# Kernel tuning notes

Measured on AMD Instinct MI355X. Metric: run time of the kernel, lower is better.

## Reference

```python
import jax, jax.numpy as jnp
import numpy as np

N = 8192
IN_F = 512
OUT_F = 128
NUM_CLASSES = 10
ALPHA = 0.2  # LeakyReLU negative slope
NEG_INF = -9e15


def setup_inputs() -> dict:
    key = jax.random.key(0)
    k_h, k_d, k_W, k_a, k_cw, k_cb = jax.random.split(key, 6)
    h = jax.random.normal(k_h, (N, IN_F), dtype=jnp.float32)
    dist = jax.random.randint(k_d, (N, N), 0, 2, dtype=jnp.int32)
    # xavier_uniform with gain=1.414
    gain = 1.414
    lim_W = gain * np.sqrt(6.0 / (IN_F + OUT_F))
    W = jax.random.uniform(k_W, (IN_F, OUT_F), minval=-lim_W, maxval=lim_W, dtype=jnp.float32)
    lim_a = gain * np.sqrt(6.0 / (2 * OUT_F + 1))
    a = jax.random.uniform(k_a, (2 * OUT_F, 1), minval=-lim_a, maxval=lim_a, dtype=jnp.float32)
    # nn.Linear(out_features, num_classes): weight [C, out], bias [C]
    lim_c = np.sqrt(1.0 / OUT_F)
    Wc = jax.random.uniform(k_cw, (NUM_CLASSES, OUT_F), minval=-lim_c, maxval=lim_c, dtype=jnp.float32)
    bc = jax.random.uniform(k_cb, (NUM_CLASSES,), minval=-lim_c, maxval=lim_c, dtype=jnp.float32)
    return {"h": h, "dist": dist, "W": W, "a": a, "Wc": Wc, "bc": bc}


def reference(h, dist, W, a, Wc, bc):
    Wh = h @ W                              # [N, out]
    Wh1 = Wh @ a[:OUT_F]                    # [N, 1]
    Wh2 = Wh @ a[OUT_F:]                    # [N, 1]
    e = jax.nn.leaky_relu(Wh1 + Wh2.T, negative_slope=ALPHA)  # [N, N]
    att = jnp.where(dist > 0, e, NEG_INF)
    att = jax.nn.softmax(att, axis=1)       # [N, N]
    h_update = jax.nn.elu(att @ Wh)         # [N, out] (dropout inactive at inference)
    y_pred = h_update @ Wc.T + bc           # [N, num_classes]
    return y_pred
```

## Files before the change

### kernel.cpp

```cpp
#include <hip/hip_runtime.h>
#include <stdint.h>

#define N 8192
#define IN_F 512
#define OUT_F 128
#define NCLS 10
#define ALPHA 0.2f

typedef float f32x4 __attribute__((ext_vector_type(4)));
typedef int   i32x4 __attribute__((ext_vector_type(4)));
typedef short s16x4 __attribute__((ext_vector_type(4)));
typedef short s16x8 __attribute__((ext_vector_type(8)));

__device__ __forceinline__ short f2bf(float x) {
    unsigned u = __builtin_bit_cast(unsigned, x);
    u = (u + 0x7FFFu + ((u >> 16) & 1u)) >> 16;
    return (short)u;
}
__device__ __forceinline__ float bf2f(short s) {
    unsigned u = ((unsigned)(unsigned short)s) << 16;
    return __builtin_bit_cast(float, u);
}

__global__ void split_w_kernel(const float* __restrict__ W,
                               short* __restrict__ WThi, short* __restrict__ WTlo) {
    int idx = blockIdx.x * 256 + threadIdx.x;
    int k = idx >> 7, col = idx & 127;
    float x = W[idx];
    short hi = f2bf(x);
    short lo = f2bf(x - bf2f(hi));
    size_t a = (size_t)(k >> 5) * (128 * 32) + (size_t)col * 32 + (k & 31);
    WThi[a] = hi;
    WTlo[a] = lo;
}

#define WH_ROWS 16
#define WH_STR 520

__global__ __launch_bounds__(256, 2)
void wh_kernel(const float* __restrict__ h, const short* __restrict__ WThi,
               const short* __restrict__ WTlo, const float* __restrict__ a,
               short* __restrict__ WhT, float* __restrict__ Wh1,
               float* __restrict__ Wh2) {
    __shared__ __align__(16) short Ahi[WH_ROWS][WH_STR];
    __shared__ __align__(16) short Alo[WH_ROWS][WH_STR];
    __shared__ __align__(16) float whs[WH_ROWS][OUT_F + 4];

    const int t = threadIdx.x;
    const int r0 = blockIdx.x * WH_ROWS;

    {
        int row = t >> 4, c4 = t & 15;
        const float* hrow = h + (size_t)(r0 + row) * IN_F;
        #pragma unroll
        for (int jj = 0; jj < 4; ++jj) {
            int k0 = c4 * 8 + jj * 128;
            f32x4 x0 = *(const f32x4*)(hrow + k0);
            f32x4 x1 = *(const f32x4*)(hrow + k0 + 4);
            s16x8 hi, lo;
            #pragma unroll
            for (int e = 0; e < 4; ++e) {
                short h0 = f2bf(x0[e]); hi[e] = h0; lo[e] = f2bf(x0[e] - bf2f(h0));
                short h1 = f2bf(x1[e]); hi[4 + e] = h1; lo[4 + e] = f2bf(x1[e] - bf2f(h1));
            }
            *(s16x8*)&Ahi[row][k0] = hi;
            *(s16x8*)&Alo[row][k0] = lo;
        }
    }
    __syncthreads();

    const int lane = t & 63, w = t >> 6;
    const int q = lane >> 4, ln16 = lane & 15;
    f32x4 acc[2] = {};
    #pragma unroll
    for (int kc = 0; kc < IN_F / 32; ++kc) {
        s16x8 ahi = *(const s16x8*)&Ahi[ln16][kc * 32 + q * 8];
        s16x8 alo = *(const s16x8*)&Alo[ln16][kc * 32 + q * 8];
        #pragma unroll
        for (int nt = 0; nt < 2; ++nt) {
            int col = w * 32 + nt * 16 + ln16;
            size_t boff = (size_t)kc * 4096 + (size_t)col * 32 + q * 8;
            s16x8 bhi = *(const s16x8*)(WThi + boff);
            s16x8 blo = *(const s16x8*)(WTlo + boff);
            acc[nt] = __builtin_amdgcn_mfma_f32_16x16x32_bf16(ahi, bhi, acc[nt], 0, 0, 0);
            acc[nt] = __builtin_amdgcn_mfma_f32_16x16x32_bf16(ahi, blo, acc[nt], 0, 0, 0);
            acc[nt] = __builtin_amdgcn_mfma_f32_16x16x32_bf16(alo, bhi, acc[nt], 0, 0, 0);
        }
    }
    #pragma unroll
    for (int nt = 0; nt < 2; ++nt)
        #pragma unroll
        for (int reg = 0; reg < 4; ++reg)
            whs[q * 4 + reg][w * 32 + nt * 16 + ln16] = acc[nt][reg];
    __syncthreads();

    if (t < 128) {
        int r = t >> 3, s = t & 7;
        float s1 = 0.f, s2 = 0.f;
        #pragma unroll
        for (int cc = 0; cc < 16; ++cc) {
            int c = s * 16 + cc;
            float v = whs[r][c];
            s1 = fmaf(v, a[c], s1);
            s2 = fmaf(v, a[OUT_F + c], s2);
        }
        s1 += __shfl_xor(s1, 1); s1 += __shfl_xor(s1, 2); s1 += __shfl_xor(s1, 4);
        s2 += __shfl_xor(s2, 1); s2 += __shfl_xor(s2, 2); s2 += __shfl_xor(s2, 4);
        if (s == 0) { Wh1[r0 + r] = s1; Wh2[r0 + r] = s2; }
    }

    {
        int c = t >> 1, h8 = t & 1;
        s16x8 pack;
        #pragma unroll
        for (int rr = 0; rr < 8; ++rr) pack[rr] = f2bf(whs[h8 * 8 + rr][c]);
        size_t addr = (size_t)(r0 >> 5) * 4096 + (size_t)c * 32 + (r0 & 16) + h8 * 8;
        *(s16x8*)(WhT + addr) = pack;
    }
}

#define BM 32
#define BK 256
#define ASTR (BK + 8)

__global__ __launch_bounds__(256, 4)
void attn_kernel(const int* __restrict__ dist, const short* __restrict__ WhT,
                 const float* __restrict__ Wh1v, const float* __restrict__ Wh2v,
                 float* __restrict__ acc_part, float* __restrict__ l_part,
                 int nit) {
    __shared__ __align__(16) short As[2][BM][ASTR];

    const int t = threadIdx.x;
    const int it = blockIdx.x & 255;
    const int sp = blockIdx.x >> 8;
    const int i0 = it * BM;
    const int r = t >> 3, s = t & 7;
    const int lane = t & 63, w = t >> 6;
    const int q = lane >> 4, ln16 = lane & 15;
    const int j0 = sp * nit * BK;

    const int* __restrict__ drow = dist + (size_t)(i0 + r) * N + j0;
    const float* __restrict__ wh2p = Wh2v + j0;
    const float wh1 = Wh1v[i0 + r];
    float l_acc = 0.f;
    f32x4 acc[2][2] = {};

    i32x4 d[8];
    #pragma unroll
    for (int u = 0; u < 8; ++u) d[u] = *(const i32x4*)(drow + u * 32 + s * 4);

    for (int kt = 0; kt < nit; ++kt) {
        const int jb = kt * BK;
        const bool more = (kt + 1) < nit;
        i32x4 dn[8];
        if (more) {
            #pragma unroll
            for (int u = 0; u < 8; ++u)
                dn[u] = *(const i32x4*)(drow + jb + BK + u * 32 + s * 4);
        }
        short* arow = &As[kt & 1][r][0];
        #pragma unroll
        for (int u = 0; u < 8; ++u) {
            f32x4 w2 = *(const f32x4*)(wh2p + jb + u * 32 + s * 4);
            s16x4 pk;
            #pragma unroll
            for (int e = 0; e < 4; ++e) {
                float sv = wh1 + w2[e];
                float lr = fmaxf(sv, ALPHA * sv);
                float pv = (d[u][e] > 0) ? __expf(lr) : 0.f;
                l_acc += pv;
                pk[e] = f2bf(pv);
            }
            *(s16x4*)(arow + u * 32 + s * 4) = pk;
        }
        __syncthreads();
        const short* ab = &As[kt & 1][0][0];
        const short* bbase = WhT + (size_t)(j0 + jb) * 128;
        #pragma unroll
        for (int kc = 0; kc < BK / 32; ++kc) {
            s16x8 a0 = *(const s16x8*)(ab + ln16 * ASTR + kc * 32 + q * 8);
            s16x8 a1 = *(const s16x8*)(ab + (16 + ln16) * ASTR + kc * 32 + q * 8);
            #pragma unroll
            for (int nt = 0; nt < 2; ++nt) {
                int col = w * 32 + nt * 16 + ln16;
                s16x8 b = *(const s16x8*)(bbase + (size_t)kc * 4096 + col * 32 + q * 8);
                acc[0][nt] = __builtin_amdgcn_mfma_f32_16x16x32_bf16(a0, b, acc[0][nt], 0, 0, 0);
                acc[1][nt] = __builtin_amdgcn_mfma_f32_16x16x32_bf16(a1, b, acc[1][nt], 0, 0, 0);
            }
        }
        if (more) {
            #pragma unroll
            for (int u = 0; u < 8; ++u) d[u] = dn[u];
        }
    }

    l_acc += __shfl_xor(l_acc, 1);
    l_acc += __shfl_xor(l_acc, 2);
    l_acc += __shfl_xor(l_acc, 4);
    if (s == 0) l_part[(size_t)sp * N + i0 + r] = l_acc;

    float* ap = acc_part + (size_t)sp * N * OUT_F + (size_t)i0 * OUT_F;
    #pragma unroll
    for (int mt = 0; mt < 2; ++mt)
        #pragma unroll
        for (int reg = 0; reg < 4; ++reg) {
            int row = mt * 16 + q * 4 + reg;
            #pragma unroll
            for (int nt = 0; nt < 2; ++nt)
                ap[(size_t)row * OUT_F + w * 32 + nt * 16 + ln16] = acc[mt][nt][reg];
        }
}

__global__ __launch_bounds__(256, 4)
void reduce_kernel(const float* __restrict__ acc_part, const float* __restrict__ l_part,
                   const float* __restrict__ Wc, const float* __restrict__ bcv,
                   float* __restrict__ out, int split) {
    __shared__ __align__(16) float hu[16][OUT_F + 4];
    const int t = threadIdx.x;
    const int i0 = blockIdx.x * 16;
    const int row = t >> 4, cg = t & 15;

    f32x4 v0 = {0.f, 0.f, 0.f, 0.f}, v1 = {0.f, 0.f, 0.f, 0.f};
    float l = 0.f;
    for (int s = 0; s < split; ++s) {
        const float* ap = acc_part + (size_t)s * N * OUT_F + (size_t)(i0 + row) * OUT_F + cg * 8;
        v0 += *(const f32x4*)ap;
        v1 += *(const f32x4*)(ap + 4);
        l += l_part[(size_t)s * N + i0 + row];
    }
    float inv = 1.f / l;
    #pragma unroll
    for (int e = 0; e < 4; ++e) {
        float x0 = v0[e] * inv; x0 = x0 > 0.f ? x0 : (__expf(x0) - 1.f);
        float x1 = v1[e] * inv; x1 = x1 > 0.f ? x1 : (__expf(x1) - 1.f);
        hu[row][cg * 8 + e] = x0;
        hu[row][cg * 8 + 4 + e] = x1;
    }
    __syncthreads();

    if (t < 16 * NCLS) {
        int rr = t / NCLS, cls = t - rr * NCLS;
        const f32x4* hurow = (const f32x4*)&hu[rr][0];
        const f32x4* wcrow = (const f32x4*)(Wc + cls * OUT_F);
        float sum = bcv[cls];
        #pragma unroll 8
        for (int c4 = 0; c4 < OUT_F / 4; ++c4) {
            f32x4 hv = hurow[c4];
            f32x4 wv = wcrow[c4];
            sum += hv[0] * wv[0] + hv[1] * wv[1] + hv[2] * wv[2] + hv[3] * wv[3];
        }
        out[(size_t)(i0 + rr) * NCLS + cls] = sum;
    }
}

extern "C" void kernel_launch(void* const* d_in, const int* in_sizes, int n_in,
                              void* d_out, int out_size, void* d_ws, size_t ws_size,
                              hipStream_t stream) {
    const float* h    = (const float*)d_in[0];
    const int*   dist = (const int*)d_in[1];
    const float* W    = (const float*)d_in[2];
    const float* a    = (const float*)d_in[3];
    const float* Wc   = (const float*)d_in[4];
    const float* bc   = (const float*)d_in[5];
    float* out = (float*)d_out;

    char* ws = (char*)d_ws;
    size_t off = 0;
    short* WhT  = (short*)(ws + off); off += (size_t)OUT_F * N * 2;
    short* WThi = (short*)(ws + off); off += (size_t)IN_F * OUT_F * 2;
    short* WTlo = (short*)(ws + off); off += (size_t)IN_F * OUT_F * 2;
    float* Wh1  = (float*)(ws + off); off += (size_t)N * 4;
    float* Wh2  = (float*)(ws + off); off += (size_t)N * 4;

    size_t per_split = (size_t)N * OUT_F * 4 + (size_t)N * 4;
    int split = 4;
    if (off + 4 * per_split > ws_size) split = 2;
    if (off + 2 * per_split > ws_size) split = 1;
    float* acc_part = (float*)(ws + off); off += (size_t)split * N * OUT_F * 4;
    float* l_part   = (float*)(ws + off);

    hipLaunchKernelGGL(split_w_kernel, dim3(256), dim3(256), 0, stream, W, WThi, WTlo);
    hipLaunchKernelGGL(wh_kernel, dim3(N / WH_ROWS), dim3(256), 0, stream,
                       h, WThi, WTlo, a, WhT, Wh1, Wh2);
    int nit = N / (BK * split);
    hipLaunchKernelGGL(attn_kernel, dim3(256 * split), dim3(256), 0, stream,
                       dist, WhT, Wh1, Wh2, acc_part, l_part, nit);
    hipLaunchKernelGGL(reduce_kernel, dim3(N / 16), dim3(256), 0, stream,
                       acc_part, l_part, Wc, bc, out, split);
}
```

Measured before the change: 441.7 us.

## Compute attention A fragments directly in registers, dropping LDS staging

The attention kernel now has each lane load the dist and Wh2 values matching its MFMA A-fragment layout and compute exp weights straight into registers. This removes the LDS tile, the __syncthreads, and the LDS reads. Each wave now owns 16 rows and all 128 output columns (8 accumulators), with a 64-row block tile, BK of 128 and a split-K of 8. The cost is losing the dist prefetch and double buffering, each wave reading the full WhT slice itself, and more partial sums for the reduce kernel.

```diff
diff --git a/kernel.cpp b/kernel.cpp
--- a/kernel.cpp
+++ b/kernel.cpp
@@ -119,96 +119,81 @@
     }
 }
 
-#define BM 32
-#define BK 256
-#define ASTR (BK + 8)
+#define BK 128
 
 __global__ __launch_bounds__(256, 4)
 void attn_kernel(const int* __restrict__ dist, const short* __restrict__ WhT,
                  const float* __restrict__ Wh1v, const float* __restrict__ Wh2v,
                  float* __restrict__ acc_part, float* __restrict__ l_part,
                  int nit) {
-    __shared__ __align__(16) short As[2][BM][ASTR];
-
     const int t = threadIdx.x;
-    const int it = blockIdx.x & 255;
-    const int sp = blockIdx.x >> 8;
-    const int i0 = it * BM;
-    const int r = t >> 3, s = t & 7;
+    const int it = blockIdx.x & 127;
+    const int sp = blockIdx.x >> 7;
+    const int i0 = it * 64;
     const int lane = t & 63, w = t >> 6;
-    const int q = lane >> 4, ln16 = lane & 15;
+    const int q = lane >> 4, m = lane & 15;
+    const int row = i0 + w * 16 + m;
     const int j0 = sp * nit * BK;
 
-    const int* __restrict__ drow = dist + (size_t)(i0 + r) * N + j0;
+    const int* __restrict__ drow = dist + (size_t)row * N + j0;
     const float* __restrict__ wh2p = Wh2v + j0;
-    const float wh1 = Wh1v[i0 + r];
+    const float wh1 = Wh1v[row];
     float l_acc = 0.f;
-    f32x4 acc[2][2] = {};
-
-    i32x4 d[8];
-    #pragma unroll
-    for (int u = 0; u < 8; ++u) d[u] = *(const i32x4*)(drow + u * 32 + s * 4);
+    f32x4 acc[8] = {};
 
     for (int kt = 0; kt < nit; ++kt) {
         const int jb = kt * BK;
-        const bool more = (kt + 1) < nit;
-        i32x4 dn[8];
-        if (more) {
-            #pragma unroll
-            for (int u = 0; u < 8; ++u)
-                dn[u] = *(const i32x4*)(drow + jb + BK + u * 32 + s * 4);
-        }
-        short* arow = &As[kt & 1][r][0];
-        #pragma unroll
-        for (int u = 0; u < 8; ++u) {
-            f32x4 w2 = *(const f32x4*)(wh2p + jb + u * 32 + s * 4);
-            s16x4 pk;
+        i32x4 d[8];
+        #pragma unroll
+        for (int kc = 0; kc < 4; ++kc) {
+            d[kc * 2]     = *(const i32x4*)(drow + jb + kc * 32 + q * 8);
+            d[kc * 2 + 1] = *(const i32x4*)(drow + jb + kc * 32 + q * 8 + 4);
+        }
+        s16x8 afr[4];
+        #pragma unroll
+        for (int kc = 0; kc < 4; ++kc) {
+            const float* w2p = wh2p + jb + kc * 32 + q * 8;
+            f32x4 w20 = *(const f32x4*)(w2p);
+            f32x4 w21 = *(const f32x4*)(w2p + 4);
             #pragma unroll
             for (int e = 0; e < 4; ++e) {
-                float sv = wh1 + w2[e];
+                float sv = wh1 + w20[e];
                 float lr = fmaxf(sv, ALPHA * sv);
-                float pv = (d[u][e] > 0) ? __expf(lr) : 0.f;
+                float pv = (d[kc * 2][e] > 0) ? __expf(lr) : 0.f;
                 l_acc += pv;
-                pk[e] = f2bf(pv);
+                unsigned u = __builtin_bit_cast(unsigned, pv);
+                afr[kc][e] = (short)((u + 0x8000u) >> 16);
+                float sv1 = wh1 + w21[e];
+                float lr1 = fmaxf(sv1, ALPHA * sv1);
+                float pv1 = (d[kc * 2 + 1][e] > 0) ? __expf(lr1) : 0.f;
+                l_acc += pv1;
+                unsigned u1 = __builtin_bit_cast(unsigned, pv1);
+                afr[kc][4 + e] = (short)((u1 + 0x8000u) >> 16);
             }
-            *(s16x4*)(arow + u * 32 + s * 4) = pk;
-        }
-        __syncthreads();
-        const short* ab = &As[kt & 1][0][0];
-        const short* bbase = WhT + (size_t)(j0 + jb) * 128;
-        #pragma unroll
-        for (int kc = 0; kc < BK / 32; ++kc) {
-            s16x8 a0 = *(const s16x8*)(ab + ln16 * ASTR + kc * 32 + q * 8);
-            s16x8 a1 = *(const s16x8*)(ab + (16 + ln16) * ASTR + kc * 32 + q * 8);
+        }
+        const short* bb = WhT + (size_t)((j0 + jb) >> 5) * 4096 + q * 8;
+        #pragma unroll
+        for (int kc = 0; kc < 4; ++kc) {
+            const short* bkc = bb + (size_t)kc * 4096;
             #pragma unroll
-            for (int nt = 0; nt < 2; ++nt) {
-                int col = w * 32 + nt * 16 + ln16;
-                s16x8 b = *(const s16x8*)(bbase + (size_t)kc * 4096 + col * 32 + q * 8);
-                acc[0][nt] = __builtin_amdgcn_mfma_f32_16x16x32_bf16(a0, b, acc[0][nt], 0, 0, 0);
-                acc[1][nt] = __builtin_amdgcn_mfma_f32_16x16x32_bf16(a1, b, acc[1][nt], 0, 0, 0);
+            for (int nt = 0; nt < 8; ++nt) {
+                s16x8 bfr = *(const s16x8*)(bkc + (nt * 16 + m) * 32);
+                acc[nt] = __builtin_amdgcn_mfma_f32_16x16x32_bf16(afr[kc], bfr, acc[nt], 0, 0, 0);
             }
         }
-        if (more) {
-            #pragma unroll
-            for (int u = 0; u < 8; ++u) d[u] = dn[u];
-        }
-    }
-
-    l_acc += __shfl_xor(l_acc, 1);
-    l_acc += __shfl_xor(l_acc, 2);
-    l_acc += __shfl_xor(l_acc, 4);
-    if (s == 0) l_part[(size_t)sp * N + i0 + r] = l_acc;
-
-    float* ap = acc_part + (size_t)sp * N * OUT_F + (size_t)i0 * OUT_F;
-    #pragma unroll
-    for (int mt = 0; mt < 2; ++mt)
-        #pragma unroll
-        for (int reg = 0; reg < 4; ++reg) {
-            int row = mt * 16 + q * 4 + reg;
-            #pragma unroll
-            for (int nt = 0; nt < 2; ++nt)
-                ap[(size_t)row * OUT_F + w * 32 + nt * 16 + ln16] = acc[mt][nt][reg];
-        }
+    }
+
+    l_acc += __shfl_xor(l_acc, 16);
+    l_acc += __shfl_xor(l_acc, 32);
+    if (q == 0) l_part[(size_t)sp * N + row] = l_acc;
+
+    float* ap = acc_part + (size_t)sp * N * OUT_F
+              + ((size_t)i0 + w * 16 + q * 4) * OUT_F + m;
+    #pragma unroll
+    for (int reg = 0; reg < 4; ++reg)
+        #pragma unroll
+        for (int nt = 0; nt < 8; ++nt)
+            ap[(size_t)reg * OUT_F + nt * 16] = acc[nt][reg];
 }
 
 __global__ __launch_bounds__(256, 4)
@@ -273,9 +258,8 @@
     float* Wh2  = (float*)(ws + off); off += (size_t)N * 4;
 
     size_t per_split = (size_t)N * OUT_F * 4 + (size_t)N * 4;
-    int split = 4;
-    if (off + 4 * per_split > ws_size) split = 2;
-    if (off + 2 * per_split > ws_size) split = 1;
+    int split = 8;
+    while (split > 1 && off + (size_t)split * per_split > ws_size) split >>= 1;
     float* acc_part = (float*)(ws + off); off += (size_t)split * N * OUT_F * 4;
     float* l_part   = (float*)(ws + off);
 
@@ -283,7 +267,7 @@
     hipLaunchKernelGGL(wh_kernel, dim3(N / WH_ROWS), dim3(256), 0, stream,
                        h, WThi, WTlo, a, WhT, Wh1, Wh2);
     int nit = N / (BK * split);
-    hipLaunchKernelGGL(attn_kernel, dim3(256 * split), dim3(256), 0, stream,
+    hipLaunchKernelGGL(attn_kernel, dim3(128 * split), dim3(256), 0, stream,
                        dist, WhT, Wh1, Wh2, acc_part, l_part, nit);
     hipLaunchKernelGGL(reduce_kernel, dim3(N / 16), dim3(256), 0, stream,
                        acc_part, l_part, Wc, bc, out, split);
```

Result: slower. 501.6 us (+13.6%).
